# Performance work log

Hardware: AMD Instinct MI355X
Metric: run time of the kernel (lower is better)

The kernel has to match this reference:

```python
import jax, jax.numpy as jnp
import numpy as np
import math

EPS = 1e-5
K = 4        # conv kernel size
N = 16       # d_state


def setup_inputs() -> dict:
    key = jax.random.key(0)
    b, l, d = 1, 2048, 1024
    di = 2 * d                      # inner channels after split
    dt_rank = math.ceil(d / 16)     # 64
    ks = jax.random.split(key, 8)
    s = 0.02
    return {
        "x": jax.random.normal(ks[0], (b, l, d), jnp.float32),
        "norm_scale": jnp.ones((d,), jnp.float32),
        "w_in": jax.random.normal(ks[1], (d, 4 * d), jnp.float32) * s,
        "conv_w": jax.random.normal(ks[2], (K, 1, di), jnp.float32) * 0.2,
        "conv_b": jnp.zeros((di,), jnp.float32),
        "A_log": jax.random.normal(ks[3], (di, N), jnp.float32) * 0.5,
        "D": jax.random.normal(ks[4], (di,), jnp.float32) * 0.1,
        "w_xproj": jax.random.normal(ks[5], (di, dt_rank + 2 * N), jnp.float32) * s,
        "w_dt": jax.random.normal(ks[6], (dt_rank, di), jnp.float32) * s,
        "b_dt": jnp.zeros((di,), jnp.float32),
        "w_out": jax.random.normal(ks[7], (di, d), jnp.float32) * s,
    }


def _causal_depthwise_conv(x, w, b):
    # x: (b,l,c), w: (K,1,c). Original pads (K-1,K-1) then slices [:, :l] == causal left-pad.
    c = x.shape[-1]
    y = jax.lax.conv_general_dilated(
        x, w, window_strides=(1,), padding=[(K - 1, 0)],
        dimension_numbers=("NWC", "WIO", "NWC"), feature_group_count=c)
    return y + b


def reference(x, norm_scale, w_in, conv_w, conv_b, A_log, D, w_xproj, w_dt, b_dt, w_out):
    dt_rank = w_dt.shape[0]
    # RMSNorm (mean=False, bias=False), scale only
    h = x * jax.lax.rsqrt(jnp.mean(x * x, axis=-1, keepdims=True) + EPS) * norm_scale
    h = h @ w_in                         # (b,l,4d)
    xs, res = jnp.split(h, 2, axis=-1)   # each (b,l,2d)
    res = jax.nn.silu(res)
    xs = jax.nn.silu(_causal_depthwise_conv(xs, conv_w, conv_b))
    proj = xs @ w_xproj                  # (b,l,dt_rank+2N)
    delta, B, C = jnp.split(proj, [dt_rank, dt_rank + N], axis=-1)
    delta = jax.nn.softplus(delta @ w_dt + b_dt)          # (b,l,c)
    A = -jnp.exp(A_log)                                   # (c,n)
    deltaA = jnp.exp(delta[..., None] * A)                # (b,l,c,n)
    deltaBx = (delta * xs)[..., None] * B[:, :, None, :]  # (b,l,c,n)

    def combine(e_i, e_j):
        a_i, b_i = e_i
        a_j, b_j = e_j
        return (a_i * a_j, a_j * b_i + b_j)

    _, ys = jax.lax.associative_scan(combine, (deltaA, deltaBx), axis=1)
    y = jnp.einsum("blcn,bln->blc", ys, C)
    out = (y + xs * D) * res
    return x + out @ w_out
```

## Files before the change

### kernel.cpp

```cpp
#include <hip/hip_runtime.h>

typedef short short8 __attribute__((ext_vector_type(8)));
typedef float floatx4 __attribute__((ext_vector_type(4)));
typedef unsigned int u32;

__device__ __forceinline__ float b2f(unsigned short u) {
    union { unsigned int i; float f; } v; v.i = ((unsigned int)u) << 16; return v.f;
}
__device__ __forceinline__ float hi2f(u32 p) {
    union { unsigned int i; float f; } v; v.i = p & 0xFFFF0000u; return v.f;
}
__device__ __forceinline__ float lo2f(u32 p) {
    union { unsigned int i; float f; } v; v.i = p << 16; return v.f;
}
__device__ __forceinline__ unsigned short f2b(float f) {
    union { unsigned int i; float f; } v; v.f = f;
    unsigned int r = v.i + 0x7FFFu + ((v.i >> 16) & 1u);
    return (unsigned short)(r >> 16);
}
__device__ __forceinline__ float ld(const void* p, size_t i, int f) {
    return f ? ((const float*)p)[i] : b2f(((const unsigned short*)p)[i]);
}
__device__ __forceinline__ void gload16(const unsigned short* g, unsigned short* l) {
    __builtin_amdgcn_global_load_lds(
        (const __attribute__((address_space(1))) u32*)(const void*)g,
        (__attribute__((address_space(3))) u32*)(void*)l, 16, 0, 0);
}
template<int CTRL>
__device__ __forceinline__ float dpp_add(float y) {
    union { float f; int i; } u, r;
    u.f = y;
    r.i = __builtin_amdgcn_update_dpp(0, u.i, CTRL, 0xF, 0xF, true);
    return y + r.f;
}

__global__ void probe_kernel(const void* scale, int* flag) {
    if (threadIdx.x == 0)
        *flag = (((const unsigned short*)scale)[0] == 0x3F80u) ? 0 : 1;
}

__global__ __launch_bounds__(256) void prep_kernel(
    const void* x, const void* scale, unsigned short* __restrict__ h,
    const void* w_in, unsigned short* __restrict__ wT, const int* flagp)
{
    const int f = *flagp;
    const int b = blockIdx.x, tid = threadIdx.x;
    if (b < 2048) {
        const int t = b;
        float xv[4];
        float ss = 0.f;
        #pragma unroll
        for (int j = 0; j < 4; j++) {
            xv[j] = ld(x, (size_t)t * 1024 + j * 256 + tid, f);
            ss += xv[j] * xv[j];
        }
        #pragma unroll
        for (int o = 32; o > 0; o >>= 1) ss += __shfl_down(ss, o);
        __shared__ float sr[4];
        if ((tid & 63) == 0) sr[tid >> 6] = ss;
        __syncthreads();
        float r = rsqrtf((sr[0] + sr[1] + sr[2] + sr[3]) * (1.f / 1024.f) + 1e-5f);
        #pragma unroll
        for (int j = 0; j < 4; j++) {
            int i = j * 256 + tid;
            h[(size_t)t * 1024 + i] = f2b(xv[j] * r * ld(scale, i, f));
        }
    } else {
        __shared__ unsigned short tile[64][68];
        const int idx = b - 2048;
        const int n0 = (idx & 63) * 64, k0 = (idx >> 6) * 64;
        #pragma unroll
        for (int j = 0; j < 16; j++) {
            int ii = tid + 256 * j, r = ii >> 6, c = ii & 63;
            tile[r][c] = f2b(ld(w_in, (size_t)(k0 + r) * 4096 + n0 + c, f));
        }
        __syncthreads();
        #pragma unroll
        for (int j = 0; j < 16; j++) {
            int ii = tid + 256 * j, r = ii >> 6, c = ii & 63;
            wT[(size_t)(n0 + r) * 1024 + k0 + c] = tile[c][r];
        }
    }
}

__global__ __launch_bounds__(256) void transpose_kernel(
    const void* W, unsigned short* __restrict__ WT, int Kdim, int Ndim, const int* flagp)
{
    const int f = *flagp;
    __shared__ unsigned short tile[64][68];
    const int k0 = blockIdx.y * 64, n0 = blockIdx.x * 64;
    const int t = threadIdx.x;
    #pragma unroll
    for (int j = 0; j < 16; j++) {
        int idx = t + 256 * j, r = idx >> 6, c = idx & 63;
        tile[r][c] = f2b(ld(W, (size_t)(k0 + r) * Ndim + n0 + c, f));
    }
    __syncthreads();
    #pragma unroll
    for (int j = 0; j < 16; j++) {
        int idx = t + 256 * j, r = idx >> 6, c = idx & 63;
        WT[(size_t)(n0 + r) * Kdim + k0 + c] = tile[c][r];
    }
}

template<int KDIM, int NDIM, int TM, int MODE>
__global__ __launch_bounds__(256) void gemm_bt_kernel(
    const unsigned short* __restrict__ A, const unsigned short* __restrict__ BT,
    void* out0, unsigned short* out1, const void* xres, const int* flagp)
{
    constexpr int RT = TM / 32;
    const int f = *flagp;
    __shared__ __align__(16) unsigned short As[TM * 64];
    __shared__ __align__(16) unsigned short Bs[64 * 64];
    const int t = threadIdx.x, w = t >> 6, lane = t & 63;
    const int q = lane >> 4, low = lane & 15;
    const int row0 = blockIdx.y * TM, n0 = blockIdx.x * 64;
    const int wy = w >> 1, wx = w & 1;

    floatx4 acc[RT][2];
    #pragma unroll
    for (int i = 0; i < RT; i++)
        #pragma unroll
        for (int j = 0; j < 2; j++) acc[i][j] = (floatx4){0.f, 0.f, 0.f, 0.f};

    const int srow = lane >> 3, scol = (lane & 7) * 8;
    const unsigned short* a_src = A + (size_t)(row0 + w * (TM / 4) + srow) * KDIM + scol;
    const unsigned short* b_src = BT + (size_t)(n0 + w * 16 + srow) * KDIM + scol;

    for (int k0 = 0; k0 < KDIM; k0 += 64) {
        #pragma unroll
        for (int i = 0; i < TM / 32; i++)
            gload16(a_src + k0 + i * 8 * KDIM, &As[(w * (TM / 4) + i * 8) * 64]);
        #pragma unroll
        for (int i = 0; i < 2; i++)
            gload16(b_src + k0 + i * 8 * KDIM, &Bs[(w * 16 + i * 8) * 64]);
        __syncthreads();
        #pragma unroll
        for (int kh = 0; kh < 2; kh++) {
            short8 af[RT];
            #pragma unroll
            for (int rt = 0; rt < RT; rt++)
                af[rt] = *(const short8*)&As[(wy * (TM / 2) + rt * 16 + low) * 64 + kh * 32 + q * 8];
            #pragma unroll
            for (int nt = 0; nt < 2; nt++) {
                short8 bf = *(const short8*)&Bs[(wx * 32 + nt * 16 + low) * 64 + kh * 32 + q * 8];
                #pragma unroll
                for (int rt = 0; rt < RT; rt++)
                    acc[rt][nt] = __builtin_amdgcn_mfma_f32_16x16x32_bf16(af[rt], bf, acc[rt][nt], 0, 0, 0);
            }
        }
        __syncthreads();
    }

    #pragma unroll
    for (int nt = 0; nt < 2; nt++) {
        const int col = n0 + wx * 32 + nt * 16 + low;
        #pragma unroll
        for (int rt = 0; rt < RT; rt++) {
            #pragma unroll
            for (int r = 0; r < 4; r++) {
                const int row = row0 + wy * (TM / 2) + rt * 16 + q * 4 + r;
                float v = acc[rt][nt][r];
                if (MODE == 0) {
                    if (col < NDIM / 2) {
                        ((unsigned short*)out0)[(size_t)row * (NDIM / 2) + col] = f2b(v);
                    } else {
                        float s = v / (1.f + __expf(-v));
                        out1[(size_t)row * (NDIM / 2) + (col - NDIM / 2)] = f2b(s);
                    }
                } else {
                    size_t idx = (size_t)row * NDIM + col;
                    float o = v + ld(xres, idx, f);
                    if (f) ((float*)out0)[idx] = o;
                    else   ((unsigned short*)out0)[idx] = f2b(o);
                }
            }
        }
    }
}

__global__ __launch_bounds__(256) void conv_kernel(
    const unsigned short* __restrict__ xs_raw, const void* conv_w,
    const void* conv_b, unsigned short* __restrict__ xs_conv, const int* flagp)
{
    const int f = *flagp;
    int id = blockIdx.x * 256 + threadIdx.x;
    int t = id >> 8, c8 = (id & 255) * 8;
    float acc[8];
    if (f) {
        const float* bf = (const float*)conv_b + c8;
        float4 b0 = *(const float4*)bf, b1 = *(const float4*)(bf + 4);
        acc[0] = b0.x; acc[1] = b0.y; acc[2] = b0.z; acc[3] = b0.w;
        acc[4] = b1.x; acc[5] = b1.y; acc[6] = b1.z; acc[7] = b1.w;
    } else {
        uint4 bv = *(const uint4*)((const unsigned short*)conv_b + c8);
        const unsigned short* bp = (const unsigned short*)&bv;
        #pragma unroll
        for (int j = 0; j < 8; j++) acc[j] = b2f(bp[j]);
    }
    #pragma unroll
    for (int k = 0; k < 4; k++) {
        int tt = t - 3 + k;
        if (tt >= 0) {
            uint4 xv = *(const uint4*)(xs_raw + (size_t)tt * 2048 + c8);
            const unsigned short* xp = (const unsigned short*)&xv;
            float wv[8];
            if (f) {
                const float* wf = (const float*)conv_w + (size_t)k * 2048 + c8;
                float4 w0 = *(const float4*)wf, w1 = *(const float4*)(wf + 4);
                wv[0] = w0.x; wv[1] = w0.y; wv[2] = w0.z; wv[3] = w0.w;
                wv[4] = w1.x; wv[5] = w1.y; wv[6] = w1.z; wv[7] = w1.w;
            } else {
                uint4 wu = *(const uint4*)((const unsigned short*)conv_w + (size_t)k * 2048 + c8);
                const unsigned short* wp = (const unsigned short*)&wu;
                #pragma unroll
                for (int j = 0; j < 8; j++) wv[j] = b2f(wp[j]);
            }
            #pragma unroll
            for (int j = 0; j < 8; j++) acc[j] += wv[j] * b2f(xp[j]);
        }
    }
    unsigned short outv[8];
    #pragma unroll
    for (int j = 0; j < 8; j++) {
        float s = acc[j] / (1.f + __expf(-acc[j]));
        outv[j] = f2b(s);
    }
    *(uint4*)(xs_conv + (size_t)t * 2048 + c8) = *(const uint4*)outv;
}

__global__ __launch_bounds__(256) void xproj_gemm_kernel(
    const unsigned short* __restrict__ A, const void* B,
    float* __restrict__ partials, const int* flagp)
{
    const int f = *flagp;
    __shared__ __align__(16) unsigned short As[64 * 32];
    __shared__ __align__(16) unsigned short Bs[64 * 32];
    const int t = threadIdx.x;
    const int row0 = blockIdx.y * 64, n0 = blockIdx.x * 64;
    const int ks = blockIdx.z;
    const int wave = t >> 6, lane = t & 63;
    const int q = lane >> 4, low = lane & 15;
    floatx4 acc[4];
    #pragma unroll
    for (int i = 0; i < 4; i++) acc[i] = (floatx4){0.f, 0.f, 0.f, 0.f};
    const int ar = t >> 2, ac = (t & 3) * 8;
    const int bk = t >> 3, bn = (t & 7) * 8;
    const int col0 = n0 + bn;
    const int kbeg = ks * 256, kend = kbeg + 256;
    for (int k0 = kbeg; k0 < kend; k0 += 32) {
        uint4 av = *(const uint4*)(A + (size_t)(row0 + ar) * 2048 + k0 + ac);
        *(uint4*)&As[ar * 32 + ac] = av;
        unsigned short bu[8];
        if (col0 < 96) {
            if (f) {
                const float* Bf = (const float*)B + (size_t)(k0 + bk) * 96 + col0;
                float4 b0 = *(const float4*)Bf, b1 = *(const float4*)(Bf + 4);
                bu[0] = f2b(b0.x); bu[1] = f2b(b0.y); bu[2] = f2b(b0.z); bu[3] = f2b(b0.w);
                bu[4] = f2b(b1.x); bu[5] = f2b(b1.y); bu[6] = f2b(b1.z); bu[7] = f2b(b1.w);
            } else {
                uint4 bv = *(const uint4*)((const unsigned short*)B + (size_t)(k0 + bk) * 96 + col0);
                *(uint4*)bu = bv;
            }
        } else {
            #pragma unroll
            for (int j = 0; j < 8; j++) bu[j] = 0;
        }
        #pragma unroll
        for (int j = 0; j < 8; j++) Bs[(bn + j) * 32 + bk] = bu[j];
        __syncthreads();
        short8 af = *(const short8*)&As[(wave * 16 + low) * 32 + q * 8];
        #pragma unroll
        for (int i = 0; i < 4; i++) {
            short8 bfr = *(const short8*)&Bs[(i * 16 + low) * 32 + q * 8];
            acc[i] = __builtin_amdgcn_mfma_f32_16x16x32_bf16(af, bfr, acc[i], 0, 0, 0);
        }
        __syncthreads();
    }
    float* out = partials + (size_t)ks * (2048 * 128);
    #pragma unroll
    for (int i = 0; i < 4; i++) {
        int col = n0 + i * 16 + low;
        #pragma unroll
        for (int r = 0; r < 4; r++) {
            int row = row0 + wave * 16 + q * 4 + r;
            out[(size_t)row * 128 + col] = acc[i][r];
        }
    }
}

__global__ __launch_bounds__(256) void xproj_reduce_kernel(
    const float* __restrict__ partials, float* __restrict__ proj)
{
    int id = blockIdx.x * 256 + threadIdx.x;
    float s = 0.f;
    #pragma unroll
    for (int k = 0; k < 8; k++) s += partials[(size_t)k * (2048 * 128) + id];
    proj[id] = s;
}

__global__ __launch_bounds__(256) void delta_gemm_kernel(
    const float* __restrict__ proj, const void* B, const void* b_dt,
    unsigned short* __restrict__ delta, const int* flagp)
{
    const int f = *flagp;
    __shared__ __align__(16) unsigned short As[64 * 32];
    __shared__ __align__(16) unsigned short Bs[64 * 32];
    const int t = threadIdx.x;
    const int row0 = blockIdx.y * 64, n0 = blockIdx.x * 64;
    const int wave = t >> 6, lane = t & 63;
    const int q = lane >> 4, low = lane & 15;
    floatx4 acc[4];
    #pragma unroll
    for (int i = 0; i < 4; i++) acc[i] = (floatx4){0.f, 0.f, 0.f, 0.f};
    const int ar = t >> 2, ac = (t & 3) * 8;
    const int bk = t >> 3, bn = (t & 7) * 8;
    #pragma unroll
    for (int k0 = 0; k0 < 64; k0 += 32) {
        const float* Ap = proj + (size_t)(row0 + ar) * 128 + k0 + ac;
        float4 a0 = *(const float4*)Ap, a1 = *(const float4*)(Ap + 4);
        As[ar * 32 + ac + 0] = f2b(a0.x); As[ar * 32 + ac + 1] = f2b(a0.y);
        As[ar * 32 + ac + 2] = f2b(a0.z); As[ar * 32 + ac + 3] = f2b(a0.w);
        As[ar * 32 + ac + 4] = f2b(a1.x); As[ar * 32 + ac + 5] = f2b(a1.y);
        As[ar * 32 + ac + 6] = f2b(a1.z); As[ar * 32 + ac + 7] = f2b(a1.w);
        unsigned short bu[8];
        if (f) {
            const float* Bp = (const float*)B + (size_t)(k0 + bk) * 2048 + n0 + bn;
            float4 b0 = *(const float4*)Bp, b1 = *(const float4*)(Bp + 4);
            bu[0] = f2b(b0.x); bu[1] = f2b(b0.y); bu[2] = f2b(b0.z); bu[3] = f2b(b0.w);
            bu[4] = f2b(b1.x); bu[5] = f2b(b1.y); bu[6] = f2b(b1.z); bu[7] = f2b(b1.w);
        } else {
            uint4 bv = *(const uint4*)((const unsigned short*)B + (size_t)(k0 + bk) * 2048 + n0 + bn);
            const unsigned short* bp = (const unsigned short*)&bv;
            #pragma unroll
            for (int j = 0; j < 8; j++) bu[j] = bp[j];
        }
        #pragma unroll
        for (int j = 0; j < 8; j++) Bs[(bn + j) * 32 + bk] = bu[j];
        __syncthreads();
        short8 af = *(const short8*)&As[(wave * 16 + low) * 32 + q * 8];
        #pragma unroll
        for (int i = 0; i < 4; i++) {
            short8 bfr = *(const short8*)&Bs[(i * 16 + low) * 32 + q * 8];
            acc[i] = __builtin_amdgcn_mfma_f32_16x16x32_bf16(af, bfr, acc[i], 0, 0, 0);
        }
        __syncthreads();
    }
    #pragma unroll
    for (int i = 0; i < 4; i++) {
        int col = n0 + i * 16 + low;
        float bias = ld(b_dt, col, f);
        #pragma unroll
        for (int r = 0; r < 4; r++) {
            int row = row0 + wave * 16 + q * 4 + r;
            float v = acc[i][r] + bias;
            float sp = fmaxf(v, 0.f) + log1pf(__expf(-fabsf(v)));
            delta[(size_t)row * 2048 + col] = f2b(sp);
        }
    }
}

__global__ __launch_bounds__(256) void scanA_kernel(
    const unsigned short* __restrict__ delta, const unsigned short* __restrict__ xs,
    const float* __restrict__ proj, const void* A_log,
    float* __restrict__ Aprod, float* __restrict__ Send, const int* flagp)
{
    const int f = *flagp;
    const int chunk = blockIdx.x, c0 = blockIdx.y * 16, t0 = chunk * 128;
    __shared__ __align__(16) u32 dxl[16 * 132];
    __shared__ __align__(16) float Bt[16 * 132];
    const int tid = threadIdx.x;
    #pragma unroll
    for (int j = 0; j < 4; j++) {
        int idx = tid + 256 * j;
        int t = idx >> 3, cp = (idx & 7) * 2;
        u32 dpair = *(const u32*)(delta + (size_t)(t0 + t) * 2048 + c0 + cp);
        u32 xpair = *(const u32*)(xs    + (size_t)(t0 + t) * 2048 + c0 + cp);
        dxl[cp * 132 + t]       = (dpair << 16) | (xpair & 0xFFFFu);
        dxl[(cp + 1) * 132 + t] = (dpair & 0xFFFF0000u) | (xpair >> 16);
    }
    #pragma unroll
    for (int j = 0; j < 8; j++) {
        int idx = tid + 256 * j;
        int t = idx >> 4, n = idx & 15;
        Bt[n * 132 + t] = proj[(size_t)(t0 + t) * 128 + 64 + n];
    }
    __syncthreads();
    const int cl = tid >> 4, n = tid & 15;
    const float A = -__expf(ld(A_log, (size_t)(c0 + cl) * 16 + n, f));
    float s = 0.f, ap = 1.f;
    for (int t4 = 0; t4 < 128; t4 += 4) {
        uint4  dx4 = *(const uint4*)&dxl[cl * 132 + t4];
        float4 b4  = *(const float4*)&Bt[n * 132 + t4];
        const u32* dxp = (const u32*)&dx4;
        const float* bp = (const float*)&b4;
        #pragma unroll
        for (int j = 0; j < 4; j++) {
            u32 p = dxp[j];
            float dv = hi2f(p), xv = lo2f(p);
            float a = __expf(dv * A);
            s = a * s + dv * xv * bp[j];
            ap *= a;
        }
    }
    size_t o = (size_t)chunk * 32768 + (size_t)c0 * 16 + tid;
    Aprod[o] = ap;
    Send[o]  = s;
}

__global__ __launch_bounds__(256) void scanB_kernel(
    const float* __restrict__ Aprod, const float* __restrict__ Send,
    float* __restrict__ prefix)
{
    int g = blockIdx.x * 256 + threadIdx.x;
    float a[16], b[16];
    #pragma unroll
    for (int k = 0; k < 16; k++) { a[k] = Aprod[(size_t)k * 32768 + g]; b[k] = Send[(size_t)k * 32768 + g]; }
    float s = 0.f;
    #pragma unroll
    for (int k = 0; k < 16; k++) { prefix[(size_t)k * 32768 + g] = s; s = a[k] * s + b[k]; }
}

__global__ __launch_bounds__(256) void scanC_kernel(
    const unsigned short* __restrict__ delta, const unsigned short* __restrict__ xs,
    const float* __restrict__ proj, const void* A_log, const void* Dv,
    const float* __restrict__ prefix, const unsigned short* __restrict__ res,
    unsigned short* __restrict__ inner, const int* flagp)
{
    const int f = *flagp;
    const int chunk = blockIdx.x, c0 = blockIdx.y * 16, t0 = chunk * 128;
    __shared__ __align__(16) u32 dxl[16 * 132];
    __shared__ __align__(16) float Bt[16 * 132];
    __shared__ __align__(16) float Ct[16 * 132];
    __shared__ __align__(16) float yl[16 * 132];
    __shared__ float Dl[16];
    const int tid = threadIdx.x;
    if (tid < 16) Dl[tid] = ld(Dv, c0 + tid, f);
    #pragma unroll
    for (int j = 0; j < 4; j++) {
        int idx = tid + 256 * j;
        int t = idx >> 3, cp = (idx & 7) * 2;
        u32 dpair = *(const u32*)(delta + (size_t)(t0 + t) * 2048 + c0 + cp);
        u32 xpair = *(const u32*)(xs    + (size_t)(t0 + t) * 2048 + c0 + cp);
        dxl[cp * 132 + t]       = (dpair << 16) | (xpair & 0xFFFFu);
        dxl[(cp + 1) * 132 + t] = (dpair & 0xFFFF0000u) | (xpair >> 16);
    }
    #pragma unroll
    for (int j = 0; j < 8; j++) {
        int idx = tid + 256 * j;
        int t = idx >> 4, n = idx & 15;
        Bt[n * 132 + t] = proj[(size_t)(t0 + t) * 128 + 64 + n];
        Ct[n * 132 + t] = proj[(size_t)(t0 + t) * 128 + 80 + n];
    }
    __syncthreads();
    const int cl = tid >> 4, n = tid & 15;
    const float A = -__expf(ld(A_log, (size_t)(c0 + cl) * 16 + n, f));
    float s = prefix[(size_t)chunk * 32768 + (size_t)c0 * 16 + tid];
    for (int t4 = 0; t4 < 128; t4 += 4) {
        uint4  dx4 = *(const uint4*)&dxl[cl * 132 + t4];
        float4 b4  = *(const float4*)&Bt[n * 132 + t4];
        float4 c4  = *(const float4*)&Ct[n * 132 + t4];
        const u32* dxp = (const u32*)&dx4;
        const float* bp = (const float*)&b4;
        const float* cp = (const float*)&c4;
        #pragma unroll
        for (int j = 0; j < 4; j++) {
            u32 p = dxp[j];
            float dv = hi2f(p), xv = lo2f(p);
            float a = __expf(dv * A);
            s = a * s + dv * xv * bp[j];
            float y = s * cp[j];
            y = dpp_add<0x111>(y);
            y = dpp_add<0x112>(y);
            y = dpp_add<0x114>(y);
            y = dpp_add<0x118>(y);
            if (n == 15) yl[cl * 132 + t4 + j] = y;
        }
    }
    __syncthreads();
    const int et = tid >> 1, ech = (tid & 1) * 8;
    size_t gbase = (size_t)(t0 + et) * 2048 + c0 + ech;
    uint4 rv4 = *(const uint4*)(res + gbase);
    const unsigned short* rp = (const unsigned short*)&rv4;
    unsigned short outv[8];
    #pragma unroll
    for (int j = 0; j < 8; j++) {
        int c = ech + j;
        float y  = yl[c * 132 + et];
        float xv = lo2f(dxl[c * 132 + et]);
        float o  = (y + xv * Dl[c]) * b2f(rp[j]);
        outv[j] = f2b(o);
    }
    *(uint4*)(inner + gbase) = *(const uint4*)outv;
}

extern "C" void kernel_launch(void* const* d_in, const int* in_sizes, int n_in,
                              void* d_out, int out_size, void* d_ws, size_t ws_size,
                              hipStream_t stream) {
    const void* x       = d_in[0];
    const void* nscale  = d_in[1];
    const void* w_in    = d_in[2];
    const void* conv_w  = d_in[3];
    const void* conv_b  = d_in[4];
    const void* A_log   = d_in[5];
    const void* Dv      = d_in[6];
    const void* w_xproj = d_in[7];
    const void* w_dt    = d_in[8];
    const void* b_dt    = d_in[9];
    const void* w_out   = d_in[10];

    char* ws = (char*)d_ws;
    int*   flag = (int*)ws;
    char* R = ws + 16384;
    unsigned short* xs_raw  = (unsigned short*)R;
    float*          Aprod   = (float*)R;
    float*          Send    = (float*)(R + 2097152);
    float*          prefix  = (float*)(R + 2 * 2097152);
    float*          proj    = (float*)(R + 3 * 2097152 + 524288);
    unsigned short* res_s   = (unsigned short*)(ws + 16384 + 8388608);
    unsigned short* xs_conv = (unsigned short*)(ws + 16384 + 2 * 8388608);
    unsigned short* delta   = (unsigned short*)(ws + 16384 + 3 * 8388608);
    unsigned short* wT      = xs_conv;
    unsigned short* h_norm  = delta;
    float*          partials= (float*)delta;
    unsigned short* woT     = delta;
    unsigned short* inner   = res_s;

    probe_kernel<<<1, 64, 0, stream>>>(nscale, flag);
    prep_kernel<<<3072, 256, 0, stream>>>(x, nscale, h_norm, w_in, wT, flag);
    gemm_bt_kernel<1024, 4096, 128, 0><<<dim3(64, 16), 256, 0, stream>>>(
        h_norm, wT, xs_raw, res_s, nullptr, flag);
    conv_kernel<<<2048, 256, 0, stream>>>(xs_raw, conv_w, conv_b, xs_conv, flag);
    xproj_gemm_kernel<<<dim3(2, 32, 8), 256, 0, stream>>>(xs_conv, w_xproj, partials, flag);
    xproj_reduce_kernel<<<1024, 256, 0, stream>>>(partials, proj);
    delta_gemm_kernel<<<dim3(32, 32), 256, 0, stream>>>(proj, w_dt, b_dt, delta, flag);
    scanA_kernel<<<dim3(16, 128), 256, 0, stream>>>(delta, xs_conv, proj, A_log, Aprod, Send, flag);
    scanB_kernel<<<128, 256, 0, stream>>>(Aprod, Send, prefix);
    scanC_kernel<<<dim3(16, 128), 256, 0, stream>>>(delta, xs_conv, proj, A_log, Dv, prefix, res_s, inner, flag);
    transpose_kernel<<<dim3(16, 32), 256, 0, stream>>>(w_out, woT, 2048, 1024, flag);
    gemm_bt_kernel<2048, 1024, 64, 1><<<dim3(16, 32), 256, 0, stream>>>(
        inner, woT, d_out, nullptr, x, flag);
}
```

Baseline: 276.3 us.

## Cut kernel launches by folding probe, scanB and w_out transpose into others

Removes the separate probe kernel by having each kernel detect the input dtype from the norm scale directly. The w_out transpose moves into the prep kernel as extra blocks, and the inter-chunk prefix scan (scanB) is folded into scanC, where each thread serially combines the earlier chunk carries. This removes three launches and the prefix buffer round trip. In exchange, later chunks of scanC do up to 15 extra dependent global loads before their main loop, and the workspace is re-laid out without aliasing.

```diff
diff --git a/kernel.cpp b/kernel.cpp
--- a/kernel.cpp
+++ b/kernel.cpp
@@ -20,6 +20,9 @@
 }
 __device__ __forceinline__ float ld(const void* p, size_t i, int f) {
     return f ? ((const float*)p)[i] : b2f(((const unsigned short*)p)[i]);
+}
+__device__ __forceinline__ int dtf(const void* scale) {
+    return (((const unsigned short*)scale)[0] == 0x3F80u) ? 0 : 1;
 }
 __device__ __forceinline__ void gload16(const unsigned short* g, unsigned short* l) {
     __builtin_amdgcn_global_load_lds(
@@ -34,16 +37,12 @@
     return y + r.f;
 }
 
-__global__ void probe_kernel(const void* scale, int* flag) {
-    if (threadIdx.x == 0)
-        *flag = (((const unsigned short*)scale)[0] == 0x3F80u) ? 0 : 1;
-}
-
 __global__ __launch_bounds__(256) void prep_kernel(
     const void* x, const void* scale, unsigned short* __restrict__ h,
-    const void* w_in, unsigned short* __restrict__ wT, const int* flagp)
-{
-    const int f = *flagp;
+    const void* w_in, unsigned short* __restrict__ wT,
+    const void* w_out, unsigned short* __restrict__ woT)
+{
+    const int f = dtf(scale);
     const int b = blockIdx.x, tid = threadIdx.x;
     if (b < 2048) {
         const int t = b;
@@ -65,7 +64,7 @@
             int i = j * 256 + tid;
             h[(size_t)t * 1024 + i] = f2b(xv[j] * r * ld(scale, i, f));
         }
-    } else {
+    } else if (b < 3072) {
         __shared__ unsigned short tile[64][68];
         const int idx = b - 2048;
         const int n0 = (idx & 63) * 64, k0 = (idx >> 6) * 64;
@@ -80,36 +79,31 @@
             int ii = tid + 256 * j, r = ii >> 6, c = ii & 63;
             wT[(size_t)(n0 + r) * 1024 + k0 + c] = tile[c][r];
         }
-    }
-}
-
-__global__ __launch_bounds__(256) void transpose_kernel(
-    const void* W, unsigned short* __restrict__ WT, int Kdim, int Ndim, const int* flagp)
-{
-    const int f = *flagp;
-    __shared__ unsigned short tile[64][68];
-    const int k0 = blockIdx.y * 64, n0 = blockIdx.x * 64;
-    const int t = threadIdx.x;
-    #pragma unroll
-    for (int j = 0; j < 16; j++) {
-        int idx = t + 256 * j, r = idx >> 6, c = idx & 63;
-        tile[r][c] = f2b(ld(W, (size_t)(k0 + r) * Ndim + n0 + c, f));
-    }
-    __syncthreads();
-    #pragma unroll
-    for (int j = 0; j < 16; j++) {
-        int idx = t + 256 * j, r = idx >> 6, c = idx & 63;
-        WT[(size_t)(n0 + r) * Kdim + k0 + c] = tile[c][r];
+    } else {
+        __shared__ unsigned short tile[64][68];
+        const int idx = b - 3072;
+        const int n0 = (idx & 15) * 64, k0 = (idx >> 4) * 64;
+        #pragma unroll
+        for (int j = 0; j < 16; j++) {
+            int ii = tid + 256 * j, r = ii >> 6, c = ii & 63;
+            tile[r][c] = f2b(ld(w_out, (size_t)(k0 + r) * 1024 + n0 + c, f));
+        }
+        __syncthreads();
+        #pragma unroll
+        for (int j = 0; j < 16; j++) {
+            int ii = tid + 256 * j, r = ii >> 6, c = ii & 63;
+            woT[(size_t)(n0 + r) * 2048 + k0 + c] = tile[c][r];
+        }
     }
 }
 
 template<int KDIM, int NDIM, int TM, int MODE>
 __global__ __launch_bounds__(256) void gemm_bt_kernel(
     const unsigned short* __restrict__ A, const unsigned short* __restrict__ BT,
-    void* out0, unsigned short* out1, const void* xres, const int* flagp)
+    void* out0, unsigned short* out1, const void* xres, const void* nscale)
 {
     constexpr int RT = TM / 32;
-    const int f = *flagp;
+    const int f = dtf(nscale);
     __shared__ __align__(16) unsigned short As[TM * 64];
     __shared__ __align__(16) unsigned short Bs[64 * 64];
     const int t = threadIdx.x, w = t >> 6, lane = t & 63;
@@ -181,9 +175,9 @@
 
 __global__ __launch_bounds__(256) void conv_kernel(
     const unsigned short* __restrict__ xs_raw, const void* conv_w,
-    const void* conv_b, unsigned short* __restrict__ xs_conv, const int* flagp)
-{
-    const int f = *flagp;
+    const void* conv_b, unsigned short* __restrict__ xs_conv, const void* nscale)
+{
+    const int f = dtf(nscale);
     int id = blockIdx.x * 256 + threadIdx.x;
     int t = id >> 8, c8 = (id & 255) * 8;
     float acc[8];
@@ -231,9 +225,9 @@
 
 __global__ __launch_bounds__(256) void xproj_gemm_kernel(
     const unsigned short* __restrict__ A, const void* B,
-    float* __restrict__ partials, const int* flagp)
-{
-    const int f = *flagp;
+    float* __restrict__ partials, const void* nscale)
+{
+    const int f = dtf(nscale);
     __shared__ __align__(16) unsigned short As[64 * 32];
     __shared__ __align__(16) unsigned short Bs[64 * 32];
     const int t = threadIdx.x;
@@ -301,9 +295,9 @@
 
 __global__ __launch_bounds__(256) void delta_gemm_kernel(
     const float* __restrict__ proj, const void* B, const void* b_dt,
-    unsigned short* __restrict__ delta, const int* flagp)
-{
-    const int f = *flagp;
+    unsigned short* __restrict__ delta, const void* nscale)
+{
+    const int f = dtf(nscale);
     __shared__ __align__(16) unsigned short As[64 * 32];
     __shared__ __align__(16) unsigned short Bs[64 * 32];
     const int t = threadIdx.x;
@@ -363,9 +357,9 @@
 __global__ __launch_bounds__(256) void scanA_kernel(
     const unsigned short* __restrict__ delta, const unsigned short* __restrict__ xs,
     const float* __restrict__ proj, const void* A_log,
-    float* __restrict__ Aprod, float* __restrict__ Send, const int* flagp)
-{
-    const int f = *flagp;
+    float* __restrict__ Aprod, float* __restrict__ Send, const void* nscale)
+{
+    const int f = dtf(nscale);
     const int chunk = blockIdx.x, c0 = blockIdx.y * 16, t0 = chunk * 128;
     __shared__ __align__(16) u32 dxl[16 * 132];
     __shared__ __align__(16) float Bt[16 * 132];
@@ -408,26 +402,14 @@
     Send[o]  = s;
 }
 
-__global__ __launch_bounds__(256) void scanB_kernel(
-    const float* __restrict__ Aprod, const float* __restrict__ Send,
-    float* __restrict__ prefix)
-{
-    int g = blockIdx.x * 256 + threadIdx.x;
-    float a[16], b[16];
-    #pragma unroll
-    for (int k = 0; k < 16; k++) { a[k] = Aprod[(size_t)k * 32768 + g]; b[k] = Send[(size_t)k * 32768 + g]; }
-    float s = 0.f;
-    #pragma unroll
-    for (int k = 0; k < 16; k++) { prefix[(size_t)k * 32768 + g] = s; s = a[k] * s + b[k]; }
-}
-
 __global__ __launch_bounds__(256) void scanC_kernel(
     const unsigned short* __restrict__ delta, const unsigned short* __restrict__ xs,
     const float* __restrict__ proj, const void* A_log, const void* Dv,
-    const float* __restrict__ prefix, const unsigned short* __restrict__ res,
-    unsigned short* __restrict__ inner, const int* flagp)
-{
-    const int f = *flagp;
+    const float* __restrict__ Aprod, const float* __restrict__ Send,
+    const unsigned short* __restrict__ res, unsigned short* __restrict__ inner,
+    const void* nscale)
+{
+    const int f = dtf(nscale);
     const int chunk = blockIdx.x, c0 = blockIdx.y * 16, t0 = chunk * 128;
     __shared__ __align__(16) u32 dxl[16 * 132];
     __shared__ __align__(16) float Bt[16 * 132];
@@ -436,6 +418,10 @@
     __shared__ float Dl[16];
     const int tid = threadIdx.x;
     if (tid < 16) Dl[tid] = ld(Dv, c0 + tid, f);
+    const int g = c0 * 16 + tid;
+    float s = 0.f;
+    for (int k = 0; k < chunk; k++)
+        s = Aprod[(size_t)k * 32768 + g] * s + Send[(size_t)k * 32768 + g];
     #pragma unroll
     for (int j = 0; j < 4; j++) {
         int idx = tid + 256 * j;
@@ -455,7 +441,6 @@
     __syncthreads();
     const int cl = tid >> 4, n = tid & 15;
     const float A = -__expf(ld(A_log, (size_t)(c0 + cl) * 16 + n, f));
-    float s = prefix[(size_t)chunk * 32768 + (size_t)c0 * 16 + tid];
     for (int t4 = 0; t4 < 128; t4 += 4) {
         uint4  dx4 = *(const uint4*)&dxl[cl * 132 + t4];
         float4 b4  = *(const float4*)&Bt[n * 132 + t4];
@@ -510,34 +495,29 @@
     const void* w_out   = d_in[10];
 
     char* ws = (char*)d_ws;
-    int*   flag = (int*)ws;
-    char* R = ws + 16384;
-    unsigned short* xs_raw  = (unsigned short*)R;
-    float*          Aprod   = (float*)R;
-    float*          Send    = (float*)(R + 2097152);
-    float*          prefix  = (float*)(R + 2 * 2097152);
-    float*          proj    = (float*)(R + 3 * 2097152 + 524288);
-    unsigned short* res_s   = (unsigned short*)(ws + 16384 + 8388608);
-    unsigned short* xs_conv = (unsigned short*)(ws + 16384 + 2 * 8388608);
-    unsigned short* delta   = (unsigned short*)(ws + 16384 + 3 * 8388608);
-    unsigned short* wT      = xs_conv;
-    unsigned short* h_norm  = delta;
-    float*          partials= (float*)delta;
-    unsigned short* woT     = delta;
+    const size_t MB = 1048576;
+    unsigned short* xs_raw  = (unsigned short*)(ws);
+    unsigned short* res_s   = (unsigned short*)(ws + 8 * MB);
+    unsigned short* xs_conv = (unsigned short*)(ws + 16 * MB);
+    unsigned short* delta   = (unsigned short*)(ws + 24 * MB);
+    unsigned short* h_norm  = (unsigned short*)(ws + 32 * MB);
+    unsigned short* wT      = (unsigned short*)(ws + 36 * MB);
+    unsigned short* woT     = (unsigned short*)(ws + 44 * MB);
+    float*          partials= (float*)(ws + 48 * MB);
+    float*          proj    = (float*)(ws + 56 * MB);
+    float*          Aprod   = (float*)(ws + 57 * MB);
+    float*          Send    = (float*)(ws + 59 * MB);
     unsigned short* inner   = res_s;
 
-    probe_kernel<<<1, 64, 0, stream>>>(nscale, flag);
-    prep_kernel<<<3072, 256, 0, stream>>>(x, nscale, h_norm, w_in, wT, flag);
+    prep_kernel<<<3584, 256, 0, stream>>>(x, nscale, h_norm, w_in, wT, w_out, woT);
     gemm_bt_kernel<1024, 4096, 128, 0><<<dim3(64, 16), 256, 0, stream>>>(
-        h_norm, wT, xs_raw, res_s, nullptr, flag);
-    conv_kernel<<<2048, 256, 0, stream>>>(xs_raw, conv_w, conv_b, xs_conv, flag);
-    xproj_gemm_kernel<<<dim3(2, 32, 8), 256, 0, stream>>>(xs_conv, w_xproj, partials, flag);
+        h_norm, wT, xs_raw, res_s, nullptr, nscale);
+    conv_kernel<<<2048, 256, 0, stream>>>(xs_raw, conv_w, conv_b, xs_conv, nscale);
+    xproj_gemm_kernel<<<dim3(2, 32, 8), 256, 0, stream>>>(xs_conv, w_xproj, partials, nscale);
     xproj_reduce_kernel<<<1024, 256, 0, stream>>>(partials, proj);
-    delta_gemm_kernel<<<dim3(32, 32), 256, 0, stream>>>(proj, w_dt, b_dt, delta, flag);
-    scanA_kernel<<<dim3(16, 128), 256, 0, stream>>>(delta, xs_conv, proj, A_log, Aprod, Send, flag);
-    scanB_kernel<<<128, 256, 0, stream>>>(Aprod, Send, prefix);
-    scanC_kernel<<<dim3(16, 128), 256, 0, stream>>>(delta, xs_conv, proj, A_log, Dv, prefix, res_s, inner, flag);
-    transpose_kernel<<<dim3(16, 32), 256, 0, stream>>>(w_out, woT, 2048, 1024, flag);
+    delta_gemm_kernel<<<dim3(32, 32), 256, 0, stream>>>(proj, w_dt, b_dt, delta, nscale);
+    scanA_kernel<<<dim3(16, 128), 256, 0, stream>>>(delta, xs_conv, proj, A_log, Aprod, Send, nscale);
+    scanC_kernel<<<dim3(16, 128), 256, 0, stream>>>(delta, xs_conv, proj, A_log, Dv, Aprod, Send, res_s, inner, nscale);
     gemm_bt_kernel<2048, 1024, 64, 1><<<dim3(16, 32), 256, 0, stream>>>(
-        inner, woT, d_out, nullptr, x, flag);
-}
+        inner, woT, d_out, nullptr, x, nscale);
+}
```

Result: faster. 270.1 us (-2.2%).
